# Kernel tuning notes

Hardware: AMD Instinct MI355X
Metric: run time of the kernel (lower is better)

## Reference

```python
import jax, jax.numpy as jnp
import numpy as np

B, N, K, D = 16, 100000, 10, 3


def setup_inputs() -> dict:
    key = jax.random.key(0)
    k1, k2, k3 = jax.random.split(key, 3)
    out = jax.random.normal(k1, (B, N, D), dtype=jnp.float32)
    target = jax.random.normal(k2, (B, N, D), dtype=jnp.float32)
    neighbor_idxs = jax.random.randint(k3, (N, K), 0, N, dtype=jnp.int32)
    neighbor_weights = jnp.full((N, K), -1.0 / K, dtype=jnp.float32)
    return {"out": out, "target": target, "neighbor_idxs": neighbor_idxs,
            "neighbor_weights": neighbor_weights}


def _laplacian(x, neighbor_idxs, neighbor_weights):
    # x: [B,N,D]; gather neighbors -> [B,N,K,D]; weighted sum over K
    gathered = x[:, neighbor_idxs]  # [B,N,K,D]
    return x + jnp.einsum('bnkd,nk->bnd', gathered, neighbor_weights)


def reference(out, target, neighbor_idxs, neighbor_weights):
    lap_out = _laplacian(out, neighbor_idxs, neighbor_weights)
    lap_target = _laplacian(target, neighbor_idxs, neighbor_weights)
    return (lap_out - lap_target) ** 2
```

## Files before the change

kernel.cpp:

```cpp
#include <hip/hip_runtime.h>


#define BB 16
#define NN 100000
#define KK 10
#define DD 3
#define TROW 48
#define NB1 160
#define NB2 160

typedef _Float16 half8 __attribute__((ext_vector_type(8)));

__global__ __launch_bounds__(256) void lap_pass1(
    const float* __restrict__ o,
    const float* __restrict__ t,
    _Float16* __restrict__ td) {
    __shared__ _Float16 tile[NB1 * TROW];
    int tid = threadIdx.x;
    size_t base = (size_t)blockIdx.x * (NB1 * DD);

#pragma unroll
    for (int ii = 0; ii < 2; ++ii) {
        int i = tid + ii * 256;
        if (i < NB1 * DD) {
            int nl = i / 3;
            int dd = i - nl * 3;
            int lo = nl * TROW + dd * 16;
            for (int b = 0; b < BB; ++b) {
                size_t rb = (size_t)b * (NN * DD) + base + i;
                tile[lo + b] = (_Float16)(o[rb] - t[rb]);
            }
        }
    }
    __syncthreads();

    const uint4* src = (const uint4*)tile;
    uint4* dst = (uint4*)(td + (size_t)blockIdx.x * (NB1 * TROW));
#pragma unroll
    for (int ii = 0; ii < 4; ++ii) {
        int i = tid + ii * 256;
        if (i < NB1 * TROW / 8) dst[i] = src[i];
    }
}

__global__ __launch_bounds__(320) void lap_pass2(
    const _Float16* __restrict__ td,
    const int* __restrict__ nidx,
    const float* __restrict__ nw,
    float* __restrict__ res) {
    int tid = threadIdx.x;
    int n = blockIdx.x * NB2 + (tid >> 1);
    int g = tid & 1;

    const half8* t8 = (const half8*)td;

    int idxs[KK];
    float wts[KK];
#pragma unroll
    for (int k = 0; k < KK; ++k) {
        idxs[k] = nidx[n * KK + k];
        wts[k] = nw[n * KK + k];
    }

    float s[DD][8];
    int base = n * 6 + g;
#pragma unroll
    for (int d = 0; d < DD; ++d) {
        half8 q = t8[base + d * 2];
#pragma unroll
        for (int i = 0; i < 8; ++i) s[d][i] = (float)q[i];
    }

#pragma unroll
    for (int k = 0; k < KK; ++k) {
        int j = idxs[k] * 6 + g;
        float w = wts[k];
#pragma unroll
        for (int d = 0; d < DD; ++d) {
            half8 q = t8[j + d * 2];
#pragma unroll
            for (int i = 0; i < 8; ++i) s[d][i] += w * (float)q[i];
        }
    }

#pragma unroll
    for (int i = 0; i < 8; ++i) {
        int b = g * 8 + i;
        size_t o = (size_t)b * (NN * DD) + (size_t)n * DD;
#pragma unroll
        for (int d = 0; d < DD; ++d) res[o + d] = s[d][i] * s[d][i];
    }
}

__global__ __launch_bounds__(256) void lap_naive(
    const float* __restrict__ out,
    const float* __restrict__ tgt,
    const int* __restrict__ nidx,
    const float* __restrict__ nw,
    float* __restrict__ res) {
    int n = blockIdx.x * blockDim.x + threadIdx.x;
    if (n >= NN) return;
    int b = blockIdx.y;
    int idxs[KK];
    float wts[KK];
#pragma unroll
    for (int k = 0; k < KK; ++k) {
        idxs[k] = nidx[n * KK + k];
        wts[k] = nw[n * KK + k];
    }
    const float* ob = out + (size_t)b * (NN * DD);
    const float* tb = tgt + (size_t)b * (NN * DD);
    int base = n * DD;
    float s0 = ob[base + 0] - tb[base + 0];
    float s1 = ob[base + 1] - tb[base + 1];
    float s2 = ob[base + 2] - tb[base + 2];
#pragma unroll
    for (int k = 0; k < KK; ++k) {
        int j = idxs[k] * DD;
        float w = wts[k];
        s0 += w * (ob[j + 0] - tb[j + 0]);
        s1 += w * (ob[j + 1] - tb[j + 1]);
        s2 += w * (ob[j + 2] - tb[j + 2]);
    }
    float* rb = res + (size_t)b * (NN * DD);
    rb[base + 0] = s0 * s0;
    rb[base + 1] = s1 * s1;
    rb[base + 2] = s2 * s2;
}

extern "C" void kernel_launch(void* const* d_in, const int* in_sizes, int n_in,
                              void* d_out, int out_size, void* d_ws, size_t ws_size,
                              hipStream_t stream) {
    const float* out = (const float*)d_in[0];
    const float* tgt = (const float*)d_in[1];
    const int* nidx = (const int*)d_in[2];
    const float* nw = (const float*)d_in[3];
    float* res = (float*)d_out;

    const size_t need = (size_t)NN * TROW * sizeof(_Float16);
    if (ws_size >= need) {
        _Float16* td = (_Float16*)d_ws;
        lap_pass1<<<NN / NB1, 256, 0, stream>>>(out, tgt, td);
        lap_pass2<<<NN / NB2, 320, 0, stream>>>(td, nidx, nw, res);
    } else {
        dim3 grid((NN + 255) / 256, BB);
        lap_naive<<<grid, dim3(256), 0, stream>>>(out, tgt, nidx, nw, res);
    }
}
```

Baseline: 40.92 us.

## Split fp16 difference table into 8 batch-pair slices for cache-local gathers

The fp16 difference table is now stored as 8 separate slices, each holding two batches (12 bytes per node), instead of one 96-byte row per node. Each pass2 thread handles one node for one slice, with the slice index taken from the block index. This makes each gathered working set 1.2 MB instead of 9.6 MB, so it fits better in L2/MALL and random neighbor gathers hit cache more often. The cost is that neighbor indices and weights are reloaded 8 times, and the gathers become 12-byte uint3 loads.

```diff
diff --git a/kernel.cpp b/kernel.cpp
--- a/kernel.cpp
+++ b/kernel.cpp
@@ -5,54 +5,61 @@
 #define NN 100000
 #define KK 10
 #define DD 3
-#define TROW 48
-#define NB1 160
-#define NB2 160
+#define NSL 8
+#define SROW 6
+#define NB1 200
+#define NB2 256
 
-typedef _Float16 half8 __attribute__((ext_vector_type(8)));
+typedef unsigned int u32;
 
 __global__ __launch_bounds__(256) void lap_pass1(
     const float* __restrict__ o,
     const float* __restrict__ t,
     _Float16* __restrict__ td) {
-    __shared__ _Float16 tile[NB1 * TROW];
+    __shared__ _Float16 tile[NSL][NB1 * SROW];
     int tid = threadIdx.x;
     size_t base = (size_t)blockIdx.x * (NB1 * DD);
 
 #pragma unroll
-    for (int ii = 0; ii < 2; ++ii) {
+    for (int ii = 0; ii < 3; ++ii) {
         int i = tid + ii * 256;
         if (i < NB1 * DD) {
             int nl = i / 3;
             int dd = i - nl * 3;
-            int lo = nl * TROW + dd * 16;
+#pragma unroll
             for (int b = 0; b < BB; ++b) {
                 size_t rb = (size_t)b * (NN * DD) + base + i;
-                tile[lo + b] = (_Float16)(o[rb] - t[rb]);
+                tile[b >> 1][nl * SROW + dd * 2 + (b & 1)] =
+                    (_Float16)(o[rb] - t[rb]);
             }
         }
     }
     __syncthreads();
 
-    const uint4* src = (const uint4*)tile;
-    uint4* dst = (uint4*)(td + (size_t)blockIdx.x * (NB1 * TROW));
+    const uint4* src = (const uint4*)&tile[0][0];
 #pragma unroll
-    for (int ii = 0; ii < 4; ++ii) {
+    for (int ii = 0; ii < 5; ++ii) {
         int i = tid + ii * 256;
-        if (i < NB1 * TROW / 8) dst[i] = src[i];
+        if (i < NSL * (NB1 * SROW / 8)) {
+            int s = i / 150;
+            int off = i - s * 150;
+            uint4* dst = (uint4*)(td + ((size_t)s * NN + (size_t)blockIdx.x * NB1) * SROW);
+            dst[off] = src[i];
+        }
     }
 }
 
-__global__ __launch_bounds__(320) void lap_pass2(
+union U3 { uint3 u; _Float16 h[6]; };
+
+__global__ __launch_bounds__(256) void lap_pass2(
     const _Float16* __restrict__ td,
     const int* __restrict__ nidx,
     const float* __restrict__ nw,
     float* __restrict__ res) {
     int tid = threadIdx.x;
-    int n = blockIdx.x * NB2 + (tid >> 1);
-    int g = tid & 1;
-
-    const half8* t8 = (const half8*)td;
+    int s = blockIdx.x & 7;
+    int n = (blockIdx.x >> 3) * NB2 + tid;
+    if (n >= NN) return;
 
     int idxs[KK];
     float wts[KK];
@@ -62,33 +69,34 @@
         wts[k] = nw[n * KK + k];
     }
 
-    float s[DD][8];
-    int base = n * 6 + g;
+    const uint3* base = (const uint3*)(td + (size_t)s * NN * SROW);
+
+    U3 self;
+    self.u = base[n];
+    float acc[SROW];
 #pragma unroll
-    for (int d = 0; d < DD; ++d) {
-        half8 q = t8[base + d * 2];
+    for (int j = 0; j < SROW; ++j) acc[j] = (float)self.h[j];
+
+    U3 q[KK];
 #pragma unroll
-        for (int i = 0; i < 8; ++i) s[d][i] = (float)q[i];
+    for (int k = 0; k < KK; ++k) q[k].u = base[idxs[k]];
+#pragma unroll
+    for (int k = 0; k < KK; ++k) {
+        float w = wts[k];
+#pragma unroll
+        for (int j = 0; j < SROW; ++j) acc[j] += w * (float)q[k].h[j];
     }
 
 #pragma unroll
-    for (int k = 0; k < KK; ++k) {
-        int j = idxs[k] * 6 + g;
-        float w = wts[k];
-#pragma unroll
-        for (int d = 0; d < DD; ++d) {
-            half8 q = t8[j + d * 2];
-#pragma unroll
-            for (int i = 0; i < 8; ++i) s[d][i] += w * (float)q[i];
-        }
-    }
-
-#pragma unroll
-    for (int i = 0; i < 8; ++i) {
-        int b = g * 8 + i;
-        size_t o = (size_t)b * (NN * DD) + (size_t)n * DD;
-#pragma unroll
-        for (int d = 0; d < DD; ++d) res[o + d] = s[d][i] * s[d][i];
+    for (int b2 = 0; b2 < 2; ++b2) {
+        int b = s * 2 + b2;
+        float* rp = res + ((size_t)b * NN + (size_t)n) * DD;
+        float v0 = acc[0 * 2 + b2];
+        float v1 = acc[1 * 2 + b2];
+        float v2 = acc[2 * 2 + b2];
+        rp[0] = v0 * v0;
+        rp[1] = v1 * v1;
+        rp[2] = v2 * v2;
     }
 }
 
@@ -137,11 +145,12 @@
     const float* nw = (const float*)d_in[3];
     float* res = (float*)d_out;
 
-    const size_t need = (size_t)NN * TROW * sizeof(_Float16);
+    const size_t need = (size_t)NSL * NN * SROW * sizeof(_Float16);
     if (ws_size >= need) {
         _Float16* td = (_Float16*)d_ws;
         lap_pass1<<<NN / NB1, 256, 0, stream>>>(out, tgt, td);
-        lap_pass2<<<NN / NB2, 320, 0, stream>>>(td, nidx, nw, res);
+        int chunks = (NN + NB2 - 1) / NB2;
+        lap_pass2<<<chunks * NSL, 256, 0, stream>>>(td, nidx, nw, res);
     } else {
         dim3 grid((NN + 255) / 256, BB);
         lap_naive<<<grid, dim3(256), 0, stream>>>(out, tgt, nidx, nw, res);
```

New measurement: 56.40 us. +37.8%, slower.

## Restructure fp16 diff layout to per-dimension planes and stage output writes through LDS

Applied to the files above, without the earlier changes.

Pass1 now has each thread convert one node directly to fp16 and write three 32-byte rows into a [D][N][B] plane layout, dropping the shared-memory transpose tile. Pass2 gathers from the per-dimension planes, issues all neighbor loads up front so more memory requests are in flight, and stages the squared results in padded LDS. It then writes coalesced float4 rows per batch instead of strided 3-float stores. The goal is to cut uncoalesced global stores and gather latency, at the cost of more registers for the prefetched neighbor data and an extra barrier.

```diff
diff --git a/kernel.cpp b/kernel.cpp
--- a/kernel.cpp
+++ b/kernel.cpp
@@ -5,9 +5,8 @@
 #define NN 100000
 #define KK 10
 #define DD 3
-#define TROW 48
-#define NB1 160
-#define NB2 160
+#define NPB 128
+#define BPAD 392
 
 typedef _Float16 half8 __attribute__((ext_vector_type(8)));
 
@@ -15,80 +14,91 @@
     const float* __restrict__ o,
     const float* __restrict__ t,
     _Float16* __restrict__ td) {
-    __shared__ _Float16 tile[NB1 * TROW];
+    int n = blockIdx.x * 256 + threadIdx.x;
+    if (n >= NN) return;
+    union { _Float16 h[BB]; uint4 u[2]; } row[DD];
+#pragma unroll
+    for (int b = 0; b < BB; ++b) {
+        size_t off = (size_t)b * (NN * DD) + (size_t)n * DD;
+        row[0].h[b] = (_Float16)(o[off + 0] - t[off + 0]);
+        row[1].h[b] = (_Float16)(o[off + 1] - t[off + 1]);
+        row[2].h[b] = (_Float16)(o[off + 2] - t[off + 2]);
+    }
+#pragma unroll
+    for (int d = 0; d < DD; ++d) {
+        uint4* dst = (uint4*)(td + ((size_t)d * NN + n) * BB);
+        dst[0] = row[d].u[0];
+        dst[1] = row[d].u[1];
+    }
+}
+
+__global__ __launch_bounds__(256) void lap_pass2(
+    const _Float16* __restrict__ td,
+    const int* __restrict__ nidx,
+    const float* __restrict__ nw,
+    float* __restrict__ res) {
+    __shared__ float tile[BB * BPAD];
     int tid = threadIdx.x;
-    size_t base = (size_t)blockIdx.x * (NB1 * DD);
+    int base = blockIdx.x * NPB;
+    int nl = tid >> 1;
+    int g = tid & 1;
+    int n = base + nl;
+    int NB = NN - base; if (NB > NPB) NB = NPB;
+
+    if (nl < NB) {
+        const half8* t8 = (const half8*)td;
+
+        int idxs[KK];
+        float wts[KK];
+#pragma unroll
+        for (int k = 0; k < KK; ++k) {
+            idxs[k] = nidx[n * KK + k];
+            wts[k] = nw[n * KK + k];
+        }
+
+        float acc[DD][8];
+#pragma unroll
+        for (int d = 0; d < DD; ++d) {
+            half8 s = t8[((size_t)d * NN + n) * 2 + g];
+#pragma unroll
+            for (int i = 0; i < 8; ++i) acc[d][i] = (float)s[i];
+        }
+
+        half8 q[KK][DD];
+#pragma unroll
+        for (int k = 0; k < KK; ++k) {
+            int j2 = idxs[k] * 2 + g;
+#pragma unroll
+            for (int d = 0; d < DD; ++d) q[k][d] = t8[(size_t)d * (NN * 2) + j2];
+        }
+#pragma unroll
+        for (int k = 0; k < KK; ++k) {
+            float w = wts[k];
+#pragma unroll
+            for (int d = 0; d < DD; ++d)
+#pragma unroll
+                for (int i = 0; i < 8; ++i) acc[d][i] += w * (float)q[k][d][i];
+        }
 
 #pragma unroll
-    for (int ii = 0; ii < 2; ++ii) {
-        int i = tid + ii * 256;
-        if (i < NB1 * DD) {
-            int nl = i / 3;
-            int dd = i - nl * 3;
-            int lo = nl * TROW + dd * 16;
-            for (int b = 0; b < BB; ++b) {
-                size_t rb = (size_t)b * (NN * DD) + base + i;
-                tile[lo + b] = (_Float16)(o[rb] - t[rb]);
+        for (int i = 0; i < 8; ++i) {
+            int b = g * 8 + i;
+#pragma unroll
+            for (int d = 0; d < DD; ++d) {
+                float v = acc[d][i];
+                tile[b * BPAD + nl * DD + d] = v * v;
             }
         }
     }
     __syncthreads();
 
-    const uint4* src = (const uint4*)tile;
-    uint4* dst = (uint4*)(td + (size_t)blockIdx.x * (NB1 * TROW));
-#pragma unroll
-    for (int ii = 0; ii < 4; ++ii) {
-        int i = tid + ii * 256;
-        if (i < NB1 * TROW / 8) dst[i] = src[i];
-    }
-}
-
-__global__ __launch_bounds__(320) void lap_pass2(
-    const _Float16* __restrict__ td,
-    const int* __restrict__ nidx,
-    const float* __restrict__ nw,
-    float* __restrict__ res) {
-    int tid = threadIdx.x;
-    int n = blockIdx.x * NB2 + (tid >> 1);
-    int g = tid & 1;
-
-    const half8* t8 = (const half8*)td;
-
-    int idxs[KK];
-    float wts[KK];
-#pragma unroll
-    for (int k = 0; k < KK; ++k) {
-        idxs[k] = nidx[n * KK + k];
-        wts[k] = nw[n * KK + k];
-    }
-
-    float s[DD][8];
-    int base = n * 6 + g;
-#pragma unroll
-    for (int d = 0; d < DD; ++d) {
-        half8 q = t8[base + d * 2];
-#pragma unroll
-        for (int i = 0; i < 8; ++i) s[d][i] = (float)q[i];
-    }
-
-#pragma unroll
-    for (int k = 0; k < KK; ++k) {
-        int j = idxs[k] * 6 + g;
-        float w = wts[k];
-#pragma unroll
-        for (int d = 0; d < DD; ++d) {
-            half8 q = t8[j + d * 2];
-#pragma unroll
-            for (int i = 0; i < 8; ++i) s[d][i] += w * (float)q[i];
-        }
-    }
-
-#pragma unroll
-    for (int i = 0; i < 8; ++i) {
-        int b = g * 8 + i;
-        size_t o = (size_t)b * (NN * DD) + (size_t)n * DD;
-#pragma unroll
-        for (int d = 0; d < DD; ++d) res[o + d] = s[d][i] * s[d][i];
+    int C4 = (NB * DD) >> 2;
+    int total = C4 * BB;
+    for (int j = tid; j < total; j += 256) {
+        int b = j / C4;
+        int pos = j - b * C4;
+        float4 v = *(const float4*)&tile[b * BPAD + pos * 4];
+        *(float4*)(res + (size_t)b * (NN * DD) + (size_t)base * DD + pos * 4) = v;
     }
 }
 
@@ -137,11 +147,11 @@
     const float* nw = (const float*)d_in[3];
     float* res = (float*)d_out;
 
-    const size_t need = (size_t)NN * TROW * sizeof(_Float16);
+    const size_t need = (size_t)DD * NN * BB * sizeof(_Float16);
     if (ws_size >= need) {
         _Float16* td = (_Float16*)d_ws;
-        lap_pass1<<<NN / NB1, 256, 0, stream>>>(out, tgt, td);
-        lap_pass2<<<NN / NB2, 320, 0, stream>>>(td, nidx, nw, res);
+        lap_pass1<<<(NN + 255) / 256, 256, 0, stream>>>(out, tgt, td);
+        lap_pass2<<<(NN + NPB - 1) / NPB, 256, 0, stream>>>(td, nidx, nw, res);
     } else {
         dim3 grid((NN + 255) / 256, BB);
         lap_naive<<<grid, dim3(256), 0, stream>>>(out, tgt, nidx, nw, res);
```

Result: slower. 51.70 us (+26.4%).
